# Optimization experiments

Measured on AMD Instinct MI355X. Metric: run time of the kernel, lower is better.

## Reference

```python
import jax, jax.numpy as jnp
import numpy as np

B, T, IN, OUT = 32, 2048, 1024, 256
DT = 1.0
TAU_MIN, TAU_MAX = 15.0, 25.0


def setup_inputs() -> dict:
    key = jax.random.key(0)
    k1, k2, k3 = jax.random.split(key, 3)
    inputs = jax.random.normal(k1, (B, T, IN), dtype=jnp.float32)
    bound = float(np.sqrt(1.0 / IN))
    weight = jax.random.uniform(k2, (OUT, IN), minval=-bound, maxval=bound, dtype=jnp.float32)
    bias = jnp.zeros((OUT,), dtype=jnp.float32)
    tau = jax.random.uniform(k3, (OUT,), minval=TAU_MIN, maxval=TAU_MAX, dtype=jnp.float32)
    decay = jnp.exp(-DT / tau)  # per-channel leak alpha in (0,1)
    return {"inputs": inputs, "weight": weight, "bias": bias, "decay": decay}


def reference(inputs, weight, bias, decay):
    # Dense projection: [B,T,IN] @ [IN,OUT] -> [B,T,OUT]
    current = jnp.einsum("bti,oi->bto", inputs, weight) + bias
    # Leaky integrator: u_t = alpha * u_{t-1} + (1-alpha) * x_t, u_0 = 0
    one_minus = 1.0 - decay

    def step(u, x):  # u,x: [B,OUT]
        u = decay * u + one_minus * x
        return u, u

    u0 = jnp.zeros((inputs.shape[0], weight.shape[0]), dtype=current.dtype)
    _, us = jax.lax.scan(step, u0, jnp.swapaxes(current, 0, 1))  # [T,B,OUT]
    return jnp.swapaxes(us, 0, 1)  # [B,T,OUT]
```

## Files before the change

### kernel.cpp

```cpp
#include <hip/hip_runtime.h>

#define B_   32
#define T_   2048
#define IN_  1024
#define OUT_ 256
#define M_   (B_ * T_)

#define BM 128
#define BN 256
#define BK 32
#define NSTEPS (IN_ / BK)
#define THREADS 512
#define TPB 16

#define LC 32
#define XPAD 264

#define ABUF_OFF(c) ((c) * (BM * BK * 2))
#define BBUF_OFF(c) (3 * (BM * BK * 2) + (c) * (BN * BK * 2))
#define XT_BYTES (BM * XPAD * 2)
#define SMEM_BYTES (XT_BYTES + 8192)

typedef __attribute__((ext_vector_type(4))) float f32x4;
typedef __attribute__((ext_vector_type(8))) __bf16 bf16x8;

__device__ __forceinline__ unsigned int f2bf_pk(float a, float b) {
    unsigned int ua = __float_as_uint(a);
    unsigned int ub = __float_as_uint(b);
    ua = (ua + 0x7fffu + ((ua >> 16) & 1u)) >> 16;
    ub = (ub + 0x7fffu + ((ub >> 16) & 1u)) >> 16;
    return ua | (ub << 16);
}
__device__ __forceinline__ unsigned short f2bf1(float a) {
    unsigned int ua = __float_as_uint(a);
    return (unsigned short)((ua + 0x7fffu + ((ua >> 16) & 1u)) >> 16);
}
__device__ __forceinline__ float bf2f(unsigned short s) {
    return __uint_as_float((unsigned int)s << 16);
}

__device__ __forceinline__ void gload_lds16(const void* g, void* l) {
    __builtin_amdgcn_global_load_lds(
        (const __attribute__((address_space(1))) void*)g,
        (__attribute__((address_space(3))) void*)l, 16, 0, 0);
}

__global__ __launch_bounds__(256) void convert_w_init(const float* __restrict__ W,
                                                      unsigned short* __restrict__ Wb,
                                                      unsigned int* __restrict__ flags) {
    const int i = blockIdx.x * 256 + threadIdx.x;
    const float4 v = ((const float4*)W)[i];
    uint2 o;
    o.x = f2bf_pk(v.x, v.y);
    o.y = f2bf_pk(v.z, v.w);
    ((uint2*)Wb)[i] = o;
    if (blockIdx.x == 0) {
        flags[threadIdx.x] = 0u;
        flags[256 + threadIdx.x] = 0u;
        if (threadIdx.x == 0) flags[512] = 0u;
    }
}

__global__ __launch_bounds__(THREADS, 4) void fused_all(
    const float* __restrict__ A, const unsigned short* __restrict__ Wb,
    const float* __restrict__ bias, const float* __restrict__ decay,
    float* __restrict__ out, float* __restrict__ localend,
    unsigned int* __restrict__ flags) {
    __shared__ __align__(16) char smem[SMEM_BYTES];
    __shared__ int s_tk;

    const int tid  = threadIdx.x;
    const int lane = tid & 63;
    const int wid  = tid >> 6;
    const int wm   = wid >> 2;
    const int wn   = wid & 3;
    const int l15  = lane & 15;
    const int l4   = lane >> 4;

    if (tid == 0) s_tk = (int)atomicAdd(&flags[512], 1u);
    __syncthreads();
    const int p    = s_tk;
    const int jb   = p & (TPB - 1);
    const int base = p - jb;
    const int bm0  = p * BM;

    const int rowA = tid >> 2;
    const int gA   = tid & 3;
    const float* gsrcA = A + (size_t)(bm0 + rowA) * IN_ + gA * 8;
    const int ldsA = rowA * BK + ((gA ^ (rowA & 3)) << 3);

    const unsigned short* gsrcB[2];
    int ldsBbase[2];
#pragma unroll
    for (int i = 0; i < 2; ++i) {
        const int q = (wid + i * 8) * 64 + lane;
        const int r = q >> 2;
        const int g = (q & 3) ^ (r & 3);
        gsrcB[i] = Wb + (size_t)r * IN_ + g * 8;
        ldsBbase[i] = (wid + i * 8) * 1024;
    }

    f32x4 acc[4][4] = {};
    float4 a0, a1;

    gload_lds16(gsrcB[0], smem + BBUF_OFF(0) + ldsBbase[0]);
    gload_lds16(gsrcB[1], smem + BBUF_OFF(0) + ldsBbase[1]);
    a0 = *(const float4*)(gsrcA);
    a1 = *(const float4*)(gsrcA + 4);
    {
        int4 w;
        w.x = f2bf_pk(a0.x, a0.y); w.y = f2bf_pk(a0.z, a0.w);
        w.z = f2bf_pk(a1.x, a1.y); w.w = f2bf_pk(a1.z, a1.w);
        *(int4*)(smem + ABUF_OFF(0) + ldsA * 2) = w;
    }
    a0 = *(const float4*)(gsrcA + BK);
    a1 = *(const float4*)(gsrcA + BK + 4);
    asm volatile("s_waitcnt lgkmcnt(0)" ::: "memory");
    __builtin_amdgcn_s_barrier();
    __builtin_amdgcn_sched_barrier(0);
    gload_lds16(gsrcB[0] + BK, smem + BBUF_OFF(1) + ldsBbase[0]);
    gload_lds16(gsrcB[1] + BK, smem + BBUF_OFF(1) + ldsBbase[1]);

    for (int i = 0; i < NSTEPS; ++i) {
        if (i + 1 < NSTEPS) {
            asm volatile("s_waitcnt vmcnt(2)" ::: "memory");
        } else {
            asm volatile("s_waitcnt vmcnt(0)" ::: "memory");
        }
        __builtin_amdgcn_sched_barrier(0);
        if (i + 1 < NSTEPS) {
            int4 w;
            w.x = f2bf_pk(a0.x, a0.y); w.y = f2bf_pk(a0.z, a0.w);
            w.z = f2bf_pk(a1.x, a1.y); w.w = f2bf_pk(a1.z, a1.w);
            *(int4*)(smem + ABUF_OFF((i + 1) % 3) + ldsA * 2) = w;
        }
        if (i + 2 < NSTEPS) {
            const int k0 = (i + 2) * BK;
            a0 = *(const float4*)(gsrcA + k0);
            a1 = *(const float4*)(gsrcA + k0 + 4);
        }
        asm volatile("s_waitcnt lgkmcnt(0)" ::: "memory");
        __builtin_amdgcn_s_barrier();
        __builtin_amdgcn_sched_barrier(0);
        if (i + 2 < NSTEPS) {
            const int k0 = (i + 2) * BK;
            gload_lds16(gsrcB[0] + k0, smem + BBUF_OFF((i + 2) % 3) + ldsBbase[0]);
            gload_lds16(gsrcB[1] + k0, smem + BBUF_OFF((i + 2) % 3) + ldsBbase[1]);
        }
        {
            const unsigned short* Ab = (const unsigned short*)(smem + ABUF_OFF(i % 3));
            const unsigned short* Bb = (const unsigned short*)(smem + BBUF_OFF(i % 3));
            bf16x8 af[4], bfv[4];
#pragma unroll
            for (int mi = 0; mi < 4; ++mi) {
                const int row = wm * 64 + mi * 16 + l15;
                af[mi] = *(const bf16x8*)&Ab[row * BK + ((l4 ^ (row & 3)) << 3)];
            }
#pragma unroll
            for (int ni = 0; ni < 4; ++ni) {
                const int col = wn * 64 + ni * 16 + l15;
                bfv[ni] = *(const bf16x8*)&Bb[col * BK + ((l4 ^ (col & 3)) << 3)];
            }
#pragma unroll
            for (int mi = 0; mi < 4; ++mi)
#pragma unroll
                for (int ni = 0; ni < 4; ++ni)
                    acc[mi][ni] = __builtin_amdgcn_mfma_f32_16x16x32_bf16(
                        af[mi], bfv[ni], acc[mi][ni], 0, 0, 0);
        }
    }
    __syncthreads();

    unsigned short* xt = (unsigned short*)smem;
    float* ceL = (float*)(smem + XT_BYTES);
    float* caL = ceL + 4 * OUT_;

#pragma unroll
    for (int ni = 0; ni < 4; ++ni) {
        const int col = wn * 64 + ni * 16 + l15;
        const float bv = bias[col];
#pragma unroll
        for (int mi = 0; mi < 4; ++mi) {
            const int r0 = wm * 64 + mi * 16 + (l4 << 2);
#pragma unroll
            for (int r = 0; r < 4; ++r)
                xt[(r0 + r) * XPAD + col] = f2bf1(acc[mi][ni][r] + bv);
        }
    }
    __syncthreads();

    for (int task = tid; task < 4 * OUT_; task += THREADS) {
        const int cl  = task >> 8;
        const int col = task & 255;
        const float alpha = decay[col];
        const float om = 1.0f - alpha;
        float u = 0.0f;
        const unsigned short* px = &xt[(cl * LC) * XPAD + col];
#pragma unroll
        for (int t = 0; t < LC; ++t)
            u = fmaf(alpha, u, om * bf2f(px[t * XPAD]));
        ceL[cl * OUT_ + col] = u;
    }
    __syncthreads();

    float alpha_c = 0.f, a32 = 0.f, a128 = 0.f;
    if (tid < OUT_) {
        alpha_c = decay[tid];
        a32 = alpha_c;
#pragma unroll
        for (int i = 1; i < LC; ++i) a32 *= alpha_c;
        const float t2 = a32 * a32;
        a128 = t2 * t2;
        float le = ceL[tid];
        le = fmaf(a32, le, ceL[OUT_ + tid]);
        le = fmaf(a32, le, ceL[2 * OUT_ + tid]);
        le = fmaf(a32, le, ceL[3 * OUT_ + tid]);
        __hip_atomic_store(&localend[(size_t)p * OUT_ + tid], le,
                           __ATOMIC_RELAXED, __HIP_MEMORY_SCOPE_AGENT);
    }
    __syncthreads();
    if (tid == 0)
        __hip_atomic_store(&flags[p], 1u, __ATOMIC_RELEASE, __HIP_MEMORY_SCOPE_AGENT);
    if (tid < jb) {
        while (__hip_atomic_load(&flags[base + tid], __ATOMIC_ACQUIRE,
                                 __HIP_MEMORY_SCOPE_AGENT) == 0u)
            __builtin_amdgcn_s_sleep(2);
    }
    __syncthreads();

    if (tid < OUT_) {
        float cin = 0.0f;
#pragma unroll
        for (int i = 0; i < TPB - 1; ++i) {
            float v = __hip_atomic_load(&localend[(size_t)(base + i) * OUT_ + tid],
                                        __ATOMIC_RELAXED, __HIP_MEMORY_SCOPE_AGENT);
            if (i < jb) cin = fmaf(a128, cin, v);
        }
        caL[tid] = cin;
        const float c1 = fmaf(a32, cin, ceL[tid]);
        const float c2 = fmaf(a32, c1, ceL[OUT_ + tid]);
        const float c3 = fmaf(a32, c2, ceL[2 * OUT_ + tid]);
        caL[OUT_ + tid] = c1;
        caL[2 * OUT_ + tid] = c2;
        caL[3 * OUT_ + tid] = c3;
    }
    __syncthreads();

    for (int task = tid; task < 4 * OUT_; task += THREADS) {
        const int cl  = task >> 8;
        const int col = task & 255;
        const float alpha = decay[col];
        const float om = 1.0f - alpha;
        float u = caL[cl * OUT_ + col];
        const unsigned short* px = &xt[(cl * LC) * XPAD + col];
        float* po = &out[(size_t)(bm0 + cl * LC) * OUT_ + col];
#pragma unroll
        for (int t = 0; t < LC; ++t) {
            u = fmaf(alpha, u, om * bf2f(px[t * XPAD]));
            po[(size_t)t * OUT_] = u;
        }
    }
}

__global__ __launch_bounds__(256) void gemm_bias(const float* __restrict__ A,
                                                 const float* __restrict__ W,
                                                 const float* __restrict__ bias,
                                                 float* __restrict__ C) {
    __shared__ float As[16][64 + 4];
    __shared__ float Ws[16][64 + 4];
    const int bm = blockIdx.y * 64;
    const int bn = blockIdx.x * 64;
    const int tid = threadIdx.x;
    const int tx = tid & 15, ty = tid >> 4;
    const int lr = tid >> 2, lc = (tid & 3) << 2;
    float acc[4][4] = {};
    const float* Ap = A + (size_t)(bm + lr) * IN_ + lc;
    const float* Wp = W + (size_t)(bn + lr) * IN_ + lc;
    for (int k0 = 0; k0 < IN_; k0 += 16) {
        const float4 a = *(const float4*)(Ap + k0);
        const float4 w = *(const float4*)(Wp + k0);
        __syncthreads();
        As[lc + 0][lr] = a.x; As[lc + 1][lr] = a.y; As[lc + 2][lr] = a.z; As[lc + 3][lr] = a.w;
        Ws[lc + 0][lr] = w.x; Ws[lc + 1][lr] = w.y; Ws[lc + 2][lr] = w.z; Ws[lc + 3][lr] = w.w;
        __syncthreads();
#pragma unroll
        for (int kk = 0; kk < 16; ++kk) {
            const float4 av = *(const float4*)&As[kk][ty << 2];
            const float4 wv = *(const float4*)&Ws[kk][tx << 2];
            const float a0[4] = {av.x, av.y, av.z, av.w};
            const float w0[4] = {wv.x, wv.y, wv.z, wv.w};
#pragma unroll
            for (int i = 0; i < 4; ++i)
#pragma unroll
                for (int j = 0; j < 4; ++j) acc[i][j] = fmaf(a0[i], w0[j], acc[i][j]);
        }
    }
#pragma unroll
    for (int i = 0; i < 4; ++i) {
        const size_t row = (size_t)(bm + (ty << 2) + i);
#pragma unroll
        for (int j = 0; j < 4; ++j)
            C[row * OUT_ + bn + (tx << 2) + j] = acc[i][j] + bias[bn + (tx << 2) + j];
    }
}

__global__ __launch_bounds__(OUT_) void scan_simple(float* __restrict__ C,
                                                    const float* __restrict__ decay) {
    const int b = blockIdx.x;
    const int o = threadIdx.x;
    const float alpha = decay[o];
    const float om = 1.0f - alpha;
    float u = 0.0f;
    float* p = C + (size_t)b * T_ * OUT_ + o;
    for (int t = 0; t < T_; ++t) {
        const float x = p[(size_t)t * OUT_];
        u = fmaf(alpha, u, om * x);
        p[(size_t)t * OUT_] = u;
    }
}

extern "C" void kernel_launch(void* const* d_in, const int* in_sizes, int n_in,
                              void* d_out, int out_size, void* d_ws, size_t ws_size,
                              hipStream_t stream) {
    const float* inputs = (const float*)d_in[0];
    const float* weight = (const float*)d_in[1];
    const float* bias   = (const float*)d_in[2];
    const float* decay  = (const float*)d_in[3];
    float* out = (float*)d_out;

    const size_t wb_bytes = (size_t)OUT_ * IN_ * 2;
    const size_t le_bytes = (size_t)(M_ / BM) * OUT_ * 4;
    const size_t fl_bytes = 4096;
    const size_t need = wb_bytes + le_bytes + fl_bytes;

    if (ws_size >= need) {
        char* w = (char*)d_ws;
        unsigned short* Wb  = (unsigned short*)w;
        float* localend     = (float*)(w + wb_bytes);
        unsigned int* flags = (unsigned int*)(w + wb_bytes + le_bytes);

        convert_w_init<<<(OUT_ * IN_ / 4) / 256, 256, 0, stream>>>(weight, Wb, flags);
        fused_all<<<M_ / BM, THREADS, 0, stream>>>(inputs, Wb, bias, decay,
                                                   out, localend, flags);
    } else {
        dim3 g(OUT_ / 64, M_ / 64);
        gemm_bias<<<g, 256, 0, stream>>>(inputs, weight, bias, out);
        scan_simple<<<B_, OUT_, 0, stream>>>(out, decay);
    }
}
```

Baseline: 113.0 us.

## Stage A in 256-wide K super-chunks with wide prefetched register loads

Replaces the per-step A load/convert/store with bulk loads of 16 float4 rows per wave covering a 256-wide K slice, converted to bf16 and written into a large swizzled LDS region reused across 8 MFMA steps. The next super-chunk's loads are issued mid-slice to overlap with compute, with vmcnt waits adjusted to match. This cuts per-step barriers and LDS writes for A and gives more coalesced global reads. In exchange it raises LDS use to 64KB+ and register pressure, and drops the occupancy hint from 4 to 2 blocks per CU.

Result: slower. 137.7 us (+21.9%).

```diff
diff --git a/kernel.cpp b/kernel.cpp
--- a/kernel.cpp
+++ b/kernel.cpp
@@ -9,17 +9,19 @@
 #define BM 128
 #define BN 256
 #define BK 32
+#define SK 256
 #define NSTEPS (IN_ / BK)
+#define NSUP (IN_ / SK)
 #define THREADS 512
 #define TPB 16
 
 #define LC 32
 #define XPAD 264
 
-#define ABUF_OFF(c) ((c) * (BM * BK * 2))
-#define BBUF_OFF(c) (3 * (BM * BK * 2) + (c) * (BN * BK * 2))
+#define ALDS_BYTES (BM * SK * 2)
+#define BBUF_OFF(c) (ALDS_BYTES + (c) * (BN * BK * 2))
 #define XT_BYTES (BM * XPAD * 2)
-#define SMEM_BYTES (XT_BYTES + 8192)
+#define SMEM_BYTES (ALDS_BYTES + 3 * (BN * BK * 2))
 
 typedef __attribute__((ext_vector_type(4))) float f32x4;
 typedef __attribute__((ext_vector_type(8))) __bf16 bf16x8;
@@ -61,7 +63,7 @@
     }
 }
 
-__global__ __launch_bounds__(THREADS, 4) void fused_all(
+__global__ __launch_bounds__(THREADS, 2) void fused_all(
     const float* __restrict__ A, const unsigned short* __restrict__ Wb,
     const float* __restrict__ bias, const float* __restrict__ decay,
     float* __restrict__ out, float* __restrict__ localend,
@@ -84,11 +86,6 @@
     const int base = p - jb;
     const int bm0  = p * BM;
 
-    const int rowA = tid >> 2;
-    const int gA   = tid & 3;
-    const float* gsrcA = A + (size_t)(bm0 + rowA) * IN_ + gA * 8;
-    const int ldsA = rowA * BK + ((gA ^ (rowA & 3)) << 3);
-
     const unsigned short* gsrcB[2];
     int ldsBbase[2];
 #pragma unroll
@@ -101,60 +98,80 @@
     }
 
     f32x4 acc[4][4] = {};
-    float4 a0, a1;
+    float4 av[16];
+
+    const float* aRow = A + (size_t)(bm0 + (wid << 4)) * IN_ + (lane << 2);
+
+    auto issueA = [&](int s) {
+        __builtin_amdgcn_sched_barrier(0);
+#pragma unroll
+        for (int j = 0; j < 16; ++j)
+            av[j] = *(const float4*)(aRow + (size_t)j * IN_ + s * SK);
+        __builtin_amdgcn_sched_barrier(0);
+    };
+    auto packA = [&]() {
+#pragma unroll
+        for (int j = 0; j < 16; ++j) {
+            const int row = (wid << 4) + j;
+            const int phys = (lane >> 1) ^ (row & 31);
+            uint2 pk;
+            pk.x = f2bf_pk(av[j].x, av[j].y);
+            pk.y = f2bf_pk(av[j].z, av[j].w);
+            *(uint2*)&smem[row * 512 + phys * 16 + (lane & 1) * 8] = pk;
+        }
+    };
 
     gload_lds16(gsrcB[0], smem + BBUF_OFF(0) + ldsBbase[0]);
     gload_lds16(gsrcB[1], smem + BBUF_OFF(0) + ldsBbase[1]);
-    a0 = *(const float4*)(gsrcA);
-    a1 = *(const float4*)(gsrcA + 4);
-    {
-        int4 w;
-        w.x = f2bf_pk(a0.x, a0.y); w.y = f2bf_pk(a0.z, a0.w);
-        w.z = f2bf_pk(a1.x, a1.y); w.w = f2bf_pk(a1.z, a1.w);
-        *(int4*)(smem + ABUF_OFF(0) + ldsA * 2) = w;
-    }
-    a0 = *(const float4*)(gsrcA + BK);
-    a1 = *(const float4*)(gsrcA + BK + 4);
+    issueA(0);
+    asm volatile("s_waitcnt vmcnt(0)" ::: "memory");
+    __builtin_amdgcn_sched_barrier(0);
+    packA();
     asm volatile("s_waitcnt lgkmcnt(0)" ::: "memory");
     __builtin_amdgcn_s_barrier();
     __builtin_amdgcn_sched_barrier(0);
     gload_lds16(gsrcB[0] + BK, smem + BBUF_OFF(1) + ldsBbase[0]);
     gload_lds16(gsrcB[1] + BK, smem + BBUF_OFF(1) + ldsBbase[1]);
 
+    const unsigned short* Alds = (const unsigned short*)smem;
+
     for (int i = 0; i < NSTEPS; ++i) {
-        if (i + 1 < NSTEPS) {
+        const int k = i & 7;
+        const int s = i >> 3;
+        if (k == 0 && i) {
+            asm volatile("s_waitcnt vmcnt(4)" ::: "memory");
+            __builtin_amdgcn_sched_barrier(0);
+            __builtin_amdgcn_s_barrier();
+            __builtin_amdgcn_sched_barrier(0);
+            packA();
+            asm volatile("s_waitcnt lgkmcnt(0)" ::: "memory");
+            __builtin_amdgcn_sched_barrier(0);
+        }
+        if (i == NSTEPS - 1) {
+            asm volatile("s_waitcnt vmcnt(0)" ::: "memory");
+        } else if (k >= 6 && s < NSUP - 1) {
+            asm volatile("s_waitcnt vmcnt(18)" ::: "memory");
+        } else {
             asm volatile("s_waitcnt vmcnt(2)" ::: "memory");
-        } else {
-            asm volatile("s_waitcnt vmcnt(0)" ::: "memory");
         }
         __builtin_amdgcn_sched_barrier(0);
-        if (i + 1 < NSTEPS) {
-            int4 w;
-            w.x = f2bf_pk(a0.x, a0.y); w.y = f2bf_pk(a0.z, a0.w);
-            w.z = f2bf_pk(a1.x, a1.y); w.w = f2bf_pk(a1.z, a1.w);
-            *(int4*)(smem + ABUF_OFF((i + 1) % 3) + ldsA * 2) = w;
-        }
-        if (i + 2 < NSTEPS) {
-            const int k0 = (i + 2) * BK;
-            a0 = *(const float4*)(gsrcA + k0);
-            a1 = *(const float4*)(gsrcA + k0 + 4);
-        }
-        asm volatile("s_waitcnt lgkmcnt(0)" ::: "memory");
         __builtin_amdgcn_s_barrier();
         __builtin_amdgcn_sched_barrier(0);
         if (i + 2 < NSTEPS) {
             const int k0 = (i + 2) * BK;
-            gload_lds16(gsrcB[0] + k0, smem + BBUF_OFF((i + 2) % 3) + ldsBbase[0]);
-            gload_lds16(gsrcB[1] + k0, smem + BBUF_OFF((i + 2) % 3) + ldsBbase[1]);
-        }
+            const int sl = (i + 2) % 3;
+            gload_lds16(gsrcB[0] + k0, smem + BBUF_OFF(sl) + ldsBbase[0]);
+            gload_lds16(gsrcB[1] + k0, smem + BBUF_OFF(sl) + ldsBbase[1]);
+        }
+        if (k == 5 && s < NSUP - 1) issueA(s + 1);
         {
-            const unsigned short* Ab = (const unsigned short*)(smem + ABUF_OFF(i % 3));
             const unsigned short* Bb = (const unsigned short*)(smem + BBUF_OFF(i % 3));
             bf16x8 af[4], bfv[4];
 #pragma unroll
             for (int mi = 0; mi < 4; ++mi) {
                 const int row = wm * 64 + mi * 16 + l15;
-                af[mi] = *(const bf16x8*)&Ab[row * BK + ((l4 ^ (row & 3)) << 3)];
+                const int g   = k * 4 + l4;
+                af[mi] = *(const bf16x8*)&Alds[row * SK + ((g ^ (row & 31)) << 3)];
             }
 #pragma unroll
             for (int ni = 0; ni < 4; ++ni) {
@@ -203,9 +220,9 @@
     }
     __syncthreads();
 
-    float alpha_c = 0.f, a32 = 0.f, a128 = 0.f;
+    float a32 = 0.f, a128 = 0.f;
     if (tid < OUT_) {
-        alpha_c = decay[tid];
+        const float alpha_c = decay[tid];
         a32 = alpha_c;
 #pragma unroll
         for (int i = 1; i < LC; ++i) a32 *= alpha_c;
```

## Replace LDS-staged GEMM pipeline with direct global-to-register MFMA loads

Applied to the files above, without the earlier changes.

Rewrites the GEMM main loop. It drops the triple-buffered LDS staging of A and B with barriers, and instead has each of four waves load its own 32 rows of A and all 256 columns of B straight from global memory into registers, then issue MFMAs with no LDS traffic or barriers. The block shrinks to 256 threads with a 2x16 accumulator tile per wave. This removes barrier and LDS overhead but makes every wave fetch the full B slice from global or L2 with little reuse, and raises register pressure.

Result: slower. 194.3 us (+71.9%).

```diff
diff --git a/kernel.cpp b/kernel.cpp
--- a/kernel.cpp
+++ b/kernel.cpp
@@ -7,17 +7,13 @@
 #define M_   (B_ * T_)
 
 #define BM 128
-#define BN 256
-#define BK 32
-#define NSTEPS (IN_ / BK)
-#define THREADS 512
+#define THREADS 256
 #define TPB 16
+#define NSTEP (IN_ / 32)
 
 #define LC 32
 #define XPAD 264
 
-#define ABUF_OFF(c) ((c) * (BM * BK * 2))
-#define BBUF_OFF(c) (3 * (BM * BK * 2) + (c) * (BN * BK * 2))
 #define XT_BYTES (BM * XPAD * 2)
 #define SMEM_BYTES (XT_BYTES + 8192)
 
@@ -37,12 +33,6 @@
 }
 __device__ __forceinline__ float bf2f(unsigned short s) {
     return __uint_as_float((unsigned int)s << 16);
-}
-
-__device__ __forceinline__ void gload_lds16(const void* g, void* l) {
-    __builtin_amdgcn_global_load_lds(
-        (const __attribute__((address_space(1))) void*)g,
-        (__attribute__((address_space(3))) void*)l, 16, 0, 0);
 }
 
 __global__ __launch_bounds__(256) void convert_w_init(const float* __restrict__ W,
@@ -61,7 +51,7 @@
     }
 }
 
-__global__ __launch_bounds__(THREADS, 4) void fused_all(
+__global__ __launch_bounds__(THREADS, 2) void fused_all(
     const float* __restrict__ A, const unsigned short* __restrict__ Wb,
     const float* __restrict__ bias, const float* __restrict__ decay,
     float* __restrict__ out, float* __restrict__ localend,
@@ -71,9 +61,7 @@
 
     const int tid  = threadIdx.x;
     const int lane = tid & 63;
-    const int wid  = tid >> 6;
-    const int wm   = wid >> 2;
-    const int wn   = wid & 3;
+    const int w    = tid >> 6;
     const int l15  = lane & 15;
     const int l4   = lane >> 4;
 
@@ -84,107 +72,58 @@
     const int base = p - jb;
     const int bm0  = p * BM;
 
-    const int rowA = tid >> 2;
-    const int gA   = tid & 3;
-    const float* gsrcA = A + (size_t)(bm0 + rowA) * IN_ + gA * 8;
-    const int ldsA = rowA * BK + ((gA ^ (rowA & 3)) << 3);
-
-    const unsigned short* gsrcB[2];
-    int ldsBbase[2];
-#pragma unroll
-    for (int i = 0; i < 2; ++i) {
-        const int q = (wid + i * 8) * 64 + lane;
-        const int r = q >> 2;
-        const int g = (q & 3) ^ (r & 3);
-        gsrcB[i] = Wb + (size_t)r * IN_ + g * 8;
-        ldsBbase[i] = (wid + i * 8) * 1024;
-    }
-
-    f32x4 acc[4][4] = {};
-    float4 a0, a1;
-
-    gload_lds16(gsrcB[0], smem + BBUF_OFF(0) + ldsBbase[0]);
-    gload_lds16(gsrcB[1], smem + BBUF_OFF(0) + ldsBbase[1]);
-    a0 = *(const float4*)(gsrcA);
-    a1 = *(const float4*)(gsrcA + 4);
-    {
-        int4 w;
-        w.x = f2bf_pk(a0.x, a0.y); w.y = f2bf_pk(a0.z, a0.w);
-        w.z = f2bf_pk(a1.x, a1.y); w.w = f2bf_pk(a1.z, a1.w);
-        *(int4*)(smem + ABUF_OFF(0) + ldsA * 2) = w;
-    }
-    a0 = *(const float4*)(gsrcA + BK);
-    a1 = *(const float4*)(gsrcA + BK + 4);
-    asm volatile("s_waitcnt lgkmcnt(0)" ::: "memory");
-    __builtin_amdgcn_s_barrier();
-    __builtin_amdgcn_sched_barrier(0);
-    gload_lds16(gsrcB[0] + BK, smem + BBUF_OFF(1) + ldsBbase[0]);
-    gload_lds16(gsrcB[1] + BK, smem + BBUF_OFF(1) + ldsBbase[1]);
-
-    for (int i = 0; i < NSTEPS; ++i) {
-        if (i + 1 < NSTEPS) {
-            asm volatile("s_waitcnt vmcnt(2)" ::: "memory");
-        } else {
-            asm volatile("s_waitcnt vmcnt(0)" ::: "memory");
-        }
-        __builtin_amdgcn_sched_barrier(0);
-        if (i + 1 < NSTEPS) {
-            int4 w;
-            w.x = f2bf_pk(a0.x, a0.y); w.y = f2bf_pk(a0.z, a0.w);
-            w.z = f2bf_pk(a1.x, a1.y); w.w = f2bf_pk(a1.z, a1.w);
-            *(int4*)(smem + ABUF_OFF((i + 1) % 3) + ldsA * 2) = w;
-        }
-        if (i + 2 < NSTEPS) {
-            const int k0 = (i + 2) * BK;
-            a0 = *(const float4*)(gsrcA + k0);
-            a1 = *(const float4*)(gsrcA + k0 + 4);
-        }
-        asm volatile("s_waitcnt lgkmcnt(0)" ::: "memory");
-        __builtin_amdgcn_s_barrier();
-        __builtin_amdgcn_sched_barrier(0);
-        if (i + 2 < NSTEPS) {
-            const int k0 = (i + 2) * BK;
-            gload_lds16(gsrcB[0] + k0, smem + BBUF_OFF((i + 2) % 3) + ldsBbase[0]);
-            gload_lds16(gsrcB[1] + k0, smem + BBUF_OFF((i + 2) % 3) + ldsBbase[1]);
-        }
-        {
-            const unsigned short* Ab = (const unsigned short*)(smem + ABUF_OFF(i % 3));
-            const unsigned short* Bb = (const unsigned short*)(smem + BBUF_OFF(i % 3));
-            bf16x8 af[4], bfv[4];
-#pragma unroll
-            for (int mi = 0; mi < 4; ++mi) {
-                const int row = wm * 64 + mi * 16 + l15;
-                af[mi] = *(const bf16x8*)&Ab[row * BK + ((l4 ^ (row & 3)) << 3)];
-            }
-#pragma unroll
-            for (int ni = 0; ni < 4; ++ni) {
-                const int col = wn * 64 + ni * 16 + l15;
-                bfv[ni] = *(const bf16x8*)&Bb[col * BK + ((l4 ^ (col & 3)) << 3)];
-            }
-#pragma unroll
-            for (int mi = 0; mi < 4; ++mi)
-#pragma unroll
-                for (int ni = 0; ni < 4; ++ni)
-                    acc[mi][ni] = __builtin_amdgcn_mfma_f32_16x16x32_bf16(
-                        af[mi], bfv[ni], acc[mi][ni], 0, 0, 0);
-        }
-    }
-    __syncthreads();
+    const float* pA0 = A + (size_t)(bm0 + w * 32 + l15) * IN_ + l4 * 8;
+    const float* pA1 = pA0 + (size_t)16 * IN_;
+    const char* WbB = (const char*)Wb + (size_t)l15 * (IN_ * 2) + l4 * 16;
+
+    f32x4 acc[2][16] = {};
+
+    float4 a00 = *(const float4*)(pA0);
+    float4 a01 = *(const float4*)(pA0 + 4);
+    float4 a10 = *(const float4*)(pA1);
+    float4 a11 = *(const float4*)(pA1 + 4);
+
+#pragma unroll 1
+    for (int k0 = 0; k0 < IN_; k0 += 32) {
+        union { uint4 u; bf16x8 v; } t0, t1;
+        t0.u.x = f2bf_pk(a00.x, a00.y); t0.u.y = f2bf_pk(a00.z, a00.w);
+        t0.u.z = f2bf_pk(a01.x, a01.y); t0.u.w = f2bf_pk(a01.z, a01.w);
+        t1.u.x = f2bf_pk(a10.x, a10.y); t1.u.y = f2bf_pk(a10.z, a10.w);
+        t1.u.z = f2bf_pk(a11.x, a11.y); t1.u.w = f2bf_pk(a11.z, a11.w);
+        const bf16x8 af0 = t0.v;
+        const bf16x8 af1 = t1.v;
+        if (k0 + 32 < IN_) {
+            a00 = *(const float4*)(pA0 + k0 + 32);
+            a01 = *(const float4*)(pA0 + k0 + 36);
+            a10 = *(const float4*)(pA1 + k0 + 32);
+            a11 = *(const float4*)(pA1 + k0 + 36);
+        }
+        const char* pb = WbB + (k0 << 1);
+        bf16x8 bfr[16];
+#pragma unroll
+        for (int n = 0; n < 16; ++n)
+            bfr[n] = *(const bf16x8*)(pb + (size_t)n * 32768);
+#pragma unroll
+        for (int n = 0; n < 16; ++n) {
+            acc[0][n] = __builtin_amdgcn_mfma_f32_16x16x32_bf16(af0, bfr[n], acc[0][n], 0, 0, 0);
+            acc[1][n] = __builtin_amdgcn_mfma_f32_16x16x32_bf16(af1, bfr[n], acc[1][n], 0, 0, 0);
+        }
+    }
 
     unsigned short* xt = (unsigned short*)smem;
     float* ceL = (float*)(smem + XT_BYTES);
     float* caL = ceL + 4 * OUT_;
 
 #pragma unroll
-    for (int ni = 0; ni < 4; ++ni) {
-        const int col = wn * 64 + ni * 16 + l15;
+    for (int n = 0; n < 16; ++n) {
+        const int col = n * 16 + l15;
         const float bv = bias[col];
 #pragma unroll
-        for (int mi = 0; mi < 4; ++mi) {
-            const int r0 = wm * 64 + mi * 16 + (l4 << 2);
+        for (int m = 0; m < 2; ++m) {
+            const int r0 = w * 32 + m * 16 + (l4 << 2);
 #pragma unroll
             for (int r = 0; r < 4; ++r)
-                xt[(r0 + r) * XPAD + col] = f2bf1(acc[mi][ni][r] + bv);
+                xt[(r0 + r) * XPAD + col] = f2bf1(acc[m][n][r] + bv);
         }
     }
     __syncthreads();
@@ -203,9 +142,9 @@
     }
     __syncthreads();
 
-    float alpha_c = 0.f, a32 = 0.f, a128 = 0.f;
+    float a32 = 0.f, a128 = 0.f;
     if (tid < OUT_) {
-        alpha_c = decay[tid];
+        const float alpha_c = decay[tid];
         a32 = alpha_c;
 #pragma unroll
         for (int i = 1; i < LC; ++i) a32 *= alpha_c;
```

## Halve GEMM row tile to 64 with 256 threads and double-buffered pipeline

Applied to the files above, without the earlier changes.

Shrinks the fused GEMM+scan block from 128 to 64 rows with 4 waves, each computing a 32x128 slab. This doubles the grid and the number of chained tiles per batch in the look-back scan. The three-stage pipeline with manual waitcnt and s_barrier becomes a simpler two-buffer loop synchronized with __syncthreads. The aim is more resident blocks and better latency hiding per CU, at the cost of more weight-tile reloads, a longer inter-block carry chain, and less overlap of loads with compute inside each block.

New measurement: 267.9 us. 137% more time.

```diff
diff --git a/kernel.cpp b/kernel.cpp
--- a/kernel.cpp
+++ b/kernel.cpp
@@ -6,20 +6,21 @@
 #define OUT_ 256
 #define M_   (B_ * T_)
 
-#define BM 128
+#define BM 64
 #define BN 256
 #define BK 32
 #define NSTEPS (IN_ / BK)
-#define THREADS 512
-#define TPB 16
+#define THREADS 256
+#define TPB (T_ / BM)
 
 #define LC 32
+#define NCHUNK 2
 #define XPAD 264
 
-#define ABUF_OFF(c) ((c) * (BM * BK * 2))
-#define BBUF_OFF(c) (3 * (BM * BK * 2) + (c) * (BN * BK * 2))
+#define ABUF_OFF(c) ((c) * 4096)
+#define BBUF_OFF(c) (8192 + (c) * 16384)
 #define XT_BYTES (BM * XPAD * 2)
-#define SMEM_BYTES (XT_BYTES + 8192)
+#define SMEM_BYTES 40960
 
 typedef __attribute__((ext_vector_type(4))) float f32x4;
 typedef __attribute__((ext_vector_type(8))) __bf16 bf16x8;
@@ -55,9 +56,9 @@
     o.y = f2bf_pk(v.z, v.w);
     ((uint2*)Wb)[i] = o;
     if (blockIdx.x == 0) {
-        flags[threadIdx.x] = 0u;
-        flags[256 + threadIdx.x] = 0u;
-        if (threadIdx.x == 0) flags[512] = 0u;
+#pragma unroll
+        for (int j = 0; j < 4; ++j) flags[j * 256 + threadIdx.x] = 0u;
+        if (threadIdx.x == 0) flags[1024] = 0u;
     }
 }
 
@@ -72,12 +73,12 @@
     const int tid  = threadIdx.x;
     const int lane = tid & 63;
     const int wid  = tid >> 6;
-    const int wm   = wid >> 2;
-    const int wn   = wid & 3;
+    const int wm   = wid >> 1;
+    const int wn   = wid & 1;
     const int l15  = lane & 15;
     const int l4   = lane >> 4;
 
-    if (tid == 0) s_tk = (int)atomicAdd(&flags[512], 1u);
+    if (tid == 0) s_tk = (int)atomicAdd(&flags[1024], 1u);
     __syncthreads();
     const int p    = s_tk;
     const int jb   = p & (TPB - 1);
@@ -89,22 +90,23 @@
     const float* gsrcA = A + (size_t)(bm0 + rowA) * IN_ + gA * 8;
     const int ldsA = rowA * BK + ((gA ^ (rowA & 3)) << 3);
 
-    const unsigned short* gsrcB[2];
-    int ldsBbase[2];
-#pragma unroll
-    for (int i = 0; i < 2; ++i) {
-        const int q = (wid + i * 8) * 64 + lane;
-        const int r = q >> 2;
-        const int g = (q & 3) ^ (r & 3);
+    const unsigned short* gsrcB[4];
+    int ldsBbase[4];
+#pragma unroll
+    for (int i = 0; i < 4; ++i) {
+        const int G = (wid * 4 + i) * 64 + lane;
+        const int r = G >> 2;
+        const int g = (G & 3) ^ (r & 3);
         gsrcB[i] = Wb + (size_t)r * IN_ + g * 8;
-        ldsBbase[i] = (wid + i * 8) * 1024;
-    }
-
-    f32x4 acc[4][4] = {};
+        ldsBbase[i] = (wid * 4 + i) * 1024;
+    }
+
+    f32x4 acc[2][8] = {};
     float4 a0, a1;
 
-    gload_lds16(gsrcB[0], smem + BBUF_OFF(0) + ldsBbase[0]);
-    gload_lds16(gsrcB[1], smem + BBUF_OFF(0) + ldsBbase[1]);
+#pragma unroll
+    for (int i = 0; i < 4; ++i)
+        gload_lds16(gsrcB[i], smem + BBUF_OFF(0) + ldsBbase[i]);
     a0 = *(const float4*)(gsrcA);
     a1 = *(const float4*)(gsrcA + 4);
     {
@@ -113,75 +115,61 @@
         w.z = f2bf_pk(a1.x, a1.y); w.w = f2bf_pk(a1.z, a1.w);
         *(int4*)(smem + ABUF_OFF(0) + ldsA * 2) = w;
     }
-    a0 = *(const float4*)(gsrcA + BK);
-    a1 = *(const float4*)(gsrcA + BK + 4);
-    asm volatile("s_waitcnt lgkmcnt(0)" ::: "memory");
-    __builtin_amdgcn_s_barrier();
-    __builtin_amdgcn_sched_barrier(0);
-    gload_lds16(gsrcB[0] + BK, smem + BBUF_OFF(1) + ldsBbase[0]);
-    gload_lds16(gsrcB[1] + BK, smem + BBUF_OFF(1) + ldsBbase[1]);
-
-    for (int i = 0; i < NSTEPS; ++i) {
-        if (i + 1 < NSTEPS) {
-            asm volatile("s_waitcnt vmcnt(2)" ::: "memory");
-        } else {
-            asm volatile("s_waitcnt vmcnt(0)" ::: "memory");
-        }
-        __builtin_amdgcn_sched_barrier(0);
-        if (i + 1 < NSTEPS) {
+    __syncthreads();
+
+    int cur = 0;
+    for (int step = 0; step < NSTEPS; ++step) {
+        const int nxt = step + 1;
+        if (nxt < NSTEPS) {
+            const int k0 = nxt * BK;
+#pragma unroll
+            for (int i = 0; i < 4; ++i)
+                gload_lds16(gsrcB[i] + k0, smem + BBUF_OFF(cur ^ 1) + ldsBbase[i]);
+            a0 = *(const float4*)(gsrcA + k0);
+            a1 = *(const float4*)(gsrcA + k0 + 4);
+        }
+        {
+            const unsigned short* Ab = (const unsigned short*)(smem + ABUF_OFF(cur));
+            const unsigned short* Bb = (const unsigned short*)(smem + BBUF_OFF(cur));
+            bf16x8 af[2], bfv[8];
+#pragma unroll
+            for (int mi = 0; mi < 2; ++mi) {
+                const int row = wm * 32 + mi * 16 + l15;
+                af[mi] = *(const bf16x8*)&Ab[row * BK + ((l4 ^ (row & 3)) << 3)];
+            }
+#pragma unroll
+            for (int ni = 0; ni < 8; ++ni) {
+                const int col = wn * 128 + ni * 16 + l15;
+                bfv[ni] = *(const bf16x8*)&Bb[col * BK + ((l4 ^ (col & 3)) << 3)];
+            }
+#pragma unroll
+            for (int mi = 0; mi < 2; ++mi)
+#pragma unroll
+                for (int ni = 0; ni < 8; ++ni)
+                    acc[mi][ni] = __builtin_amdgcn_mfma_f32_16x16x32_bf16(
+                        af[mi], bfv[ni], acc[mi][ni], 0, 0, 0);
+        }
+        if (nxt < NSTEPS) {
             int4 w;
             w.x = f2bf_pk(a0.x, a0.y); w.y = f2bf_pk(a0.z, a0.w);
             w.z = f2bf_pk(a1.x, a1.y); w.w = f2bf_pk(a1.z, a1.w);
-            *(int4*)(smem + ABUF_OFF((i + 1) % 3) + ldsA * 2) = w;
-        }
-        if (i + 2 < NSTEPS) {
-            const int k0 = (i + 2) * BK;
-            a0 = *(const float4*)(gsrcA + k0);
-            a1 = *(const float4*)(gsrcA + k0 + 4);
-        }
-        asm volatile("s_waitcnt lgkmcnt(0)" ::: "memory");
-        __builtin_amdgcn_s_barrier();
-        __builtin_amdgcn_sched_barrier(0);
-        if (i + 2 < NSTEPS) {
-            const int k0 = (i + 2) * BK;
-            gload_lds16(gsrcB[0] + k0, smem + BBUF_OFF((i + 2) % 3) + ldsBbase[0]);
-            gload_lds16(gsrcB[1] + k0, smem + BBUF_OFF((i + 2) % 3) + ldsBbase[1]);
-        }
-        {
-            const unsigned short* Ab = (const unsigned short*)(smem + ABUF_OFF(i % 3));
-            const unsigned short* Bb = (const unsigned short*)(smem + BBUF_OFF(i % 3));
-            bf16x8 af[4], bfv[4];
-#pragma unroll
-            for (int mi = 0; mi < 4; ++mi) {
-                const int row = wm * 64 + mi * 16 + l15;
-                af[mi] = *(const bf16x8*)&Ab[row * BK + ((l4 ^ (row & 3)) << 3)];
-            }
-#pragma unroll
-            for (int ni = 0; ni < 4; ++ni) {
-                const int col = wn * 64 + ni * 16 + l15;
-                bfv[ni] = *(const bf16x8*)&Bb[col * BK + ((l4 ^ (col & 3)) << 3)];
-            }
-#pragma unroll
-            for (int mi = 0; mi < 4; ++mi)
-#pragma unroll
-                for (int ni = 0; ni < 4; ++ni)
-                    acc[mi][ni] = __builtin_amdgcn_mfma_f32_16x16x32_bf16(
-                        af[mi], bfv[ni], acc[mi][ni], 0, 0, 0);
-        }
-    }
-    __syncthreads();
+            *(int4*)(smem + ABUF_OFF(cur ^ 1) + ldsA * 2) = w;
+        }
+        __syncthreads();
+        cur ^= 1;
+    }
 
     unsigned short* xt = (unsigned short*)smem;
     float* ceL = (float*)(smem + XT_BYTES);
-    float* caL = ceL + 4 * OUT_;
-
-#pragma unroll
-    for (int ni = 0; ni < 4; ++ni) {
-        const int col = wn * 64 + ni * 16 + l15;
+    float* caL = ceL + NCHUNK * OUT_;
+
+#pragma unroll
+    for (int ni = 0; ni < 8; ++ni) {
+        const int col = wn * 128 + ni * 16 + l15;
         const float bv = bias[col];
 #pragma unroll
-        for (int mi = 0; mi < 4; ++mi) {
-            const int r0 = wm * 64 + mi * 16 + (l4 << 2);
+        for (int mi = 0; mi < 2; ++mi) {
+            const int r0 = wm * 32 + mi * 16 + (l4 << 2);
 #pragma unroll
             for (int r = 0; r < 4; ++r)
                 xt[(r0 + r) * XPAD + col] = f2bf1(acc[mi][ni][r] + bv);
@@ -189,7 +177,7 @@
     }
     __syncthreads();
 
-    for (int task = tid; task < 4 * OUT_; task += THREADS) {
+    for (int task = tid; task < NCHUNK * OUT_; task += THREADS) {
         const int cl  = task >> 8;
         const int col = task & 255;
         const float alpha = decay[col];
@@ -203,18 +191,15 @@
     }
     __syncthreads();
 
-    float alpha_c = 0.f, a32 = 0.f, a128 = 0.f;
+    float a32 = 0.f, a64 = 0.f;
     if (tid < OUT_) {
-        alpha_c = decay[tid];
+        const float alpha_c = decay[tid];
         a32 = alpha_c;
 #pragma unroll
         for (int i = 1; i < LC; ++i) a32 *= alpha_c;
-        const float t2 = a32 * a32;
-        a128 = t2 * t2;
+        a64 = a32 * a32;
         float le = ceL[tid];
         le = fmaf(a32, le, ceL[OUT_ + tid]);
-        le = fmaf(a32, le, ceL[2 * OUT_ + tid]);
-        le = fmaf(a32, le, ceL[3 * OUT_ + tid]);
         __hip_atomic_store(&localend[(size_t)p * OUT_ + tid], le,
                            __ATOMIC_RELAXED, __HIP_MEMORY_SCOPE_AGENT);
     }
@@ -234,19 +219,14 @@
         for (int i = 0; i < TPB - 1; ++i) {
             float v = __hip_atomic_load(&localend[(size_t)(base + i) * OUT_ + tid],
                                         __ATOMIC_RELAXED, __HIP_MEMORY_SCOPE_AGENT);
-            if (i < jb) cin = fmaf(a128, cin, v);
+            if (i < jb) cin = fmaf(a64, cin, v);
         }
         caL[tid] = cin;
-        const float c1 = fmaf(a32, cin, ceL[tid]);
-        const float c2 = fmaf(a32, c1, ceL[OUT_ + tid]);
-        const float c3 = fmaf(a32, c2, ceL[2 * OUT_ + tid]);
-        caL[OUT_ + tid] = c1;
-        caL[2 * OUT_ + tid] = c2;
-        caL[3 * OUT_ + tid] = c3;
-    }
-    __syncthreads();
-
-    for (int task = tid; task < 4 * OUT_; task += THREADS) {
+        caL[OUT_ + tid] = fmaf(a32, cin, ceL[tid]);
+    }
+    __syncthreads();
+
+    for (int task = tid; task < NCHUNK * OUT_; task += THREADS) {
         const int cl  = task >> 8;
         const int col = task & 255;
         const float alpha = decay[col];
@@ -330,7 +310,7 @@
 
     const size_t wb_bytes = (size_t)OUT_ * IN_ * 2;
     const size_t le_bytes = (size_t)(M_ / BM) * OUT_ * 4;
-    const size_t fl_bytes = 4096;
+    const size_t fl_bytes = 8192;
     const size_t need = wb_bytes + le_bytes + fl_bytes;
 
     if (ws_size >= need) {
```
